# Performance work log

Measured on AMD Instinct MI355X. Metric: run time of the kernel, lower is better.

Reference implementation:

```python
import math
import jax, jax.numpy as jnp
import numpy as np
from jax import lax

# ---- static config (mirrors RPN init + typical torchvision anchor setup) ----
IMG_H = IMG_W = 800
LEVELS = [(200, 200, 4, 32), (100, 100, 8, 64), (50, 50, 16, 128), (25, 25, 32, 256), (13, 13, 64, 512)]  # (h, w, stride, anchor_size)
RATIOS = (0.5, 1.0, 2.0)
COUNTS = tuple(h * w * len(RATIOS) for (h, w, _, _) in LEVELS)  # (120000,30000,7500,1875,507)
A_TOTAL = sum(COUNTS)  # 159882
PRE_NMS = 2000
POST_NMS = 1000
NMS_THRESH = 0.7
MIN_SIZE = 1e-3
BBOX_CLIP = math.log(1000.0 / 16)


def make_anchors():
    parts = []
    for (h, w, stride, size) in LEVELS:
        ws = np.array([size * np.sqrt(1.0 / r) for r in RATIOS], np.float32)  # [3]
        hs = np.array([size * np.sqrt(r) for r in RATIOS], np.float32)
        sx = (np.arange(w, dtype=np.float32) + 0.5) * stride
        sy = (np.arange(h, dtype=np.float32) + 0.5) * stride
        cy, cx = np.meshgrid(sy, sx, indexing='ij')
        cx = cx.reshape(-1, 1)
        cy = cy.reshape(-1, 1)
        a = np.stack([cx - ws / 2, cy - hs / 2, cx + ws / 2, cy + hs / 2], axis=-1)  # [HW,3,4]
        parts.append(a.reshape(-1, 4))
    return np.concatenate(parts, 0).astype(np.float32)


def setup_inputs() -> dict:
    key = jax.random.key(0)
    k1, k2 = jax.random.split(key)
    scores = jax.random.normal(k1, (1, A_TOTAL), dtype=jnp.float32)
    deltas = jax.random.normal(k2, (A_TOTAL, 4), dtype=jnp.float32) * 0.5
    anchors = jnp.asarray(make_anchors())
    return {'scores': scores, 'deltas': deltas, 'anchors': anchors}


def _pairwise_iou(b):
    area = (b[:, 2] - b[:, 0]) * (b[:, 3] - b[:, 1])  # [K]
    lt = jnp.maximum(b[:, None, :2], b[None, :, :2])   # [K,K,2]
    rb = jnp.minimum(b[:, None, 2:], b[None, :, 2:])
    wh = jnp.maximum(rb - lt, 0.0)
    inter = wh[..., 0] * wh[..., 1]
    return inter / (area[:, None] + area[None, :] - inter)


def reference(scores, deltas, anchors):
    s_all = lax.stop_gradient(scores[0])  # original does cls.detach()
    # ---- box decode (torchvision-style) ----
    w = anchors[:, 2] - anchors[:, 0]
    h = anchors[:, 3] - anchors[:, 1]
    cx = anchors[:, 0] + 0.5 * w
    cy = anchors[:, 1] + 0.5 * h
    dx, dy = deltas[:, 0], deltas[:, 1]
    dw = jnp.minimum(deltas[:, 2], BBOX_CLIP)
    dh = jnp.minimum(deltas[:, 3], BBOX_CLIP)
    px = cx + dx * w
    py = cy + dy * h
    pw = jnp.exp(dw) * w
    ph = jnp.exp(dh) * h
    boxes = jnp.stack([px - 0.5 * pw, py - 0.5 * ph, px + 0.5 * pw, py + 0.5 * ph], axis=1)  # [A,4]
    # ---- per-level top-k over objectness ----
    idx_parts = []
    off = 0
    for c in COUNTS:
        k = min(PRE_NMS, c)
        _, ti = lax.top_k(lax.dynamic_slice_in_dim(s_all, off, c), k)
        idx_parts.append(ti + off)
        off += c
    top_idx = jnp.concatenate(idx_parts)  # [K=8382]
    K = top_idx.shape[0]
    s = s_all[top_idx]
    b = boxes[top_idx]
    # ---- clip to image + min-size validity (masked instead of compacted) ----
    b = jnp.stack([jnp.clip(b[:, 0], 0.0, IMG_W), jnp.clip(b[:, 1], 0.0, IMG_H),
                   jnp.clip(b[:, 2], 0.0, IMG_W), jnp.clip(b[:, 3], 0.0, IMG_H)], axis=1)
    valid = ((b[:, 2] - b[:, 0]) >= MIN_SIZE) & ((b[:, 3] - b[:, 1]) >= MIN_SIZE)
    # ---- per-level NMS offset; replicates original feature_mask[keep] indexing
    # (positional indexing into the full anchor-order level-id vector) ----
    fmask_full = np.concatenate([np.full(c, i, np.float32) for i, c in enumerate(COUNTS)])
    fmask = jnp.asarray(fmask_full[:K])
    box_max = jnp.max(jnp.where(valid[:, None], b, -jnp.inf))
    bn = b + (fmask * (box_max + 1.0))[:, None]
    # ---- greedy NMS on score-sorted candidates ----
    s_m = jnp.where(valid, s, -jnp.inf)
    order = jnp.argsort(-s_m)
    s_srt = s_m[order]
    b_srt = b[order]
    iou = _pairwise_iou(bn[order])  # [K,K] ~281MB
    ar = jnp.arange(K)

    def body(i, keep):
        sup = (iou[i] > NMS_THRESH) & (ar > i)
        return jnp.where(keep[i], keep & ~sup, keep)

    keep = lax.fori_loop(0, K, body, s_srt > -jnp.inf)
    final = jnp.where(keep, s_srt, -jnp.inf)
    out_s, oidx = lax.top_k(final, POST_NMS)  # top post_nms kept, score order; -inf pads
    out_b = b_srt[oidx]
    return out_b, out_s
```

## Files before the change

### kernel.cpp

```cpp
#include <hip/hip_runtime.h>
#include <math.h>

typedef unsigned int u32;
typedef unsigned long long u64;
typedef unsigned char u8;

#define K_TOT 8382
#define NCH 131
#define CAP 1024
#define EC 64
#define DC 8
#define GCAP 32768
#define IMGSZ 800.0f

__device__ __constant__ int LOFF[5] = {0, 120000, 150000, 157500, 159375};
__device__ __constant__ int LCNT[5] = {120000, 30000, 7500, 1875, 507};
__device__ __constant__ int KSEL[5] = {2000, 2000, 2000, 1875, 507};
__device__ __constant__ int SELB[5] = {0, 2000, 4000, 6000, 7875};
__device__ __constant__ int HBS[4] = {0, 118, 148, 156};
__device__ __constant__ int GBS[6] = {0, 118, 148, 156, 158, 159};

static __device__ __forceinline__ u32 fkey(float x) {
    u32 u = __float_as_uint(x);
    u32 m = (u32)(((int)u) >> 31) | 0x80000000u;
    return u ^ m;
}

static __device__ __forceinline__ int lvl_of(int s) {
    return (s < 2000) ? 0 : (s < 4000) ? 1 : (s < 6000) ? 2 : (s < 7875) ? 3 : 4;
}

static __device__ __forceinline__ u32 rdl32(u32 v, int j) {
    return (u32)__builtin_amdgcn_readlane((int)v, j);
}
static __device__ __forceinline__ u64 rdlane64(u64 v, int j) {
    u32 lo = (u32)__builtin_amdgcn_readlane((int)(u32)v, j);
    u32 hi = (u32)__builtin_amdgcn_readlane((int)(u32)(v >> 32), j);
    return ((u64)hi << 32) | (u64)lo;
}

static __device__ __forceinline__ u32 wor32(u32 x) {
    x |= (u32)__builtin_amdgcn_update_dpp(0, (int)x, 0x111, 0xf, 0xf, true);
    x |= (u32)__builtin_amdgcn_update_dpp(0, (int)x, 0x112, 0xf, 0xf, true);
    x |= (u32)__builtin_amdgcn_update_dpp(0, (int)x, 0x114, 0xf, 0xf, true);
    x |= (u32)__builtin_amdgcn_update_dpp(0, (int)x, 0x118, 0xf, 0xf, true);
    x |= (u32)__builtin_amdgcn_update_dpp(0, (int)x, 0x142, 0xa, 0xf, true);
    x |= (u32)__builtin_amdgcn_update_dpp(0, (int)x, 0x143, 0xc, 0xf, true);
    return x;
}

static __device__ __forceinline__ u64 pullkeep(u64 k0, u64 k1, u64 k2, u32 sch) {
    int bidx = (int)((sch & 63u) << 2);
    u32 a0l = (u32)__builtin_amdgcn_ds_bpermute(bidx, (int)(u32)k0);
    u32 a0h = (u32)__builtin_amdgcn_ds_bpermute(bidx, (int)(u32)(k0 >> 32));
    u32 a1l = (u32)__builtin_amdgcn_ds_bpermute(bidx, (int)(u32)k1);
    u32 a1h = (u32)__builtin_amdgcn_ds_bpermute(bidx, (int)(u32)(k1 >> 32));
    u32 a2l = (u32)__builtin_amdgcn_ds_bpermute(bidx, (int)(u32)k2);
    u32 a2h = (u32)__builtin_amdgcn_ds_bpermute(bidx, (int)(u32)(k2 >> 32));
    return (sch < 64) ? (((u64)a0h << 32) | (u64)a0l)
         : (sch < 128) ? (((u64)a1h << 32) | (u64)a1l)
                       : (((u64)a2h << 32) | (u64)a2l);
}

static __device__ __forceinline__ void thresh_scan(const u32* hist, u32* scanbuf, int m,
                                                   u32 need, u32* sv, int t) {
    for (int i = t; i < m; i += 1024) scanbuf[i] = hist[m - 1 - i];
    __syncthreads();
    for (int ofs = 1; ofs < m; ofs <<= 1) {
        int i0 = t, i1 = t + 1024;
        u32 a0 = 0, a1 = 0;
        if (i0 < m && i0 >= ofs) a0 = scanbuf[i0 - ofs];
        if (i1 < m && i1 >= ofs) a1 = scanbuf[i1 - ofs];
        __syncthreads();
        if (i0 < m && i0 >= ofs) scanbuf[i0] += a0;
        if (i1 < m && i1 >= ofs) scanbuf[i1] += a1;
        __syncthreads();
    }
    for (int i = t; i < m; i += 1024) {
        u32 inc = scanbuf[i];
        u32 exc = i ? scanbuf[i - 1] : 0;
        if (inc >= need && exc < need) { sv[0] = (u32)(m - 1 - i); sv[1] = need - exc; }
    }
    __syncthreads();
}

__global__ __launch_bounds__(1024) void k_hist(const float* __restrict__ scores,
                                               u32* __restrict__ hist3) {
    __shared__ u32 lh[2048];
    int t = threadIdx.x;
    lh[t] = 0; lh[t + 1024] = 0;
    __syncthreads();
    int b = blockIdx.x;
    int l = (b < HBS[1]) ? 0 : (b < HBS[2]) ? 1 : 2;
    int i = (b - HBS[l]) * 1024 + t;
    if (i < LCNT[l]) atomicAdd(&lh[fkey(scores[LOFF[l] + i]) >> 21], 1u);
    __syncthreads();
    u32* h = hist3 + l * 2048;
    if (lh[t]) atomicAdd(&h[t], lh[t]);
    if (lh[t + 1024]) atomicAdd(&h[t + 1024], lh[t + 1024]);
}

__global__ __launch_bounds__(1024) void k_thresh(const u32* __restrict__ hist3,
                                                 u32* __restrict__ tinfo) {
    __shared__ u32 scanbuf[2048];
    __shared__ u32 sv[2];
    int l = blockIdx.x;
    int t = threadIdx.x;
    thresh_scan(hist3 + l * 2048, scanbuf, 2048, (u32)KSEL[l], sv, t);
    if (t == 0) { tinfo[l * 2] = sv[0]; tinfo[l * 2 + 1] = sv[1]; }
}

__global__ __launch_bounds__(1024) void k_gather(const float* __restrict__ scores,
                                                 const u32* __restrict__ tinfo,
                                                 u32* __restrict__ sel, u32* __restrict__ cgt,
                                                 u32* __restrict__ gcnt, u32* __restrict__ gidx,
                                                 u32* __restrict__ gkey) {
    int b = blockIdx.x;
    int l = (b < GBS[1]) ? 0 : (b < GBS[2]) ? 1 : (b < GBS[3]) ? 2 : (b < GBS[4]) ? 3 : 4;
    int i = (b - GBS[l]) * 1024 + threadIdx.x;
    if (i >= LCNT[l]) return;
    int off = LOFF[l], sb = SELB[l];
    if (l >= 3) { sel[sb + i] = (u32)(off + i); return; }
    u32 ky = fkey(scores[off + i]);
    u32 b1 = tinfo[l * 2];
    u32 top = ky >> 21;
    if (top > b1) {
        u32 p = atomicAdd(&cgt[l], 1u);
        sel[sb + p] = (u32)(off + i);
    } else if (top == b1) {
        u32 e = atomicAdd(&gcnt[l], 1u);
        if (e < GCAP) { gidx[l * GCAP + e] = (u32)i; gkey[l * GCAP + e] = ky; }
    }
}

__global__ __launch_bounds__(1024) void k_final(const u32* __restrict__ gidx,
                                                const u32* __restrict__ gkey,
                                                const u32* __restrict__ gcnt,
                                                const u32* __restrict__ tinfo,
                                                u32* __restrict__ sel) {
    __shared__ u32 hist[2048];
    __shared__ u32 scanbuf[2048];
    __shared__ u32 eqbuf[1024];
    __shared__ u32 sv[2];
    __shared__ u32 c2, ceq;
    int l = blockIdx.x;
    int t = threadIdx.x;
    int k = KSEL[l], sb = SELB[l], off = LOFF[l];
    u32 m = gcnt[l]; if (m > GCAP) m = GCAP;
    u32 b1 = tinfo[l * 2];
    u32 need = tinfo[l * 2 + 1];
    const u32* kb = gkey + l * GCAP;
    const u32* ib = gidx + l * GCAP;
    hist[t] = 0; hist[t + 1024] = 0; __syncthreads();
    for (u32 e = t; e < m; e += 1024) atomicAdd(&hist[(kb[e] >> 10) & 2047u], 1u);
    __syncthreads();
    thresh_scan(hist, scanbuf, 2048, need, sv, t);
    u32 b2 = sv[0], need2 = sv[1];
    __syncthreads();
    hist[t] = 0; __syncthreads();
    for (u32 e = t; e < m; e += 1024) {
        u32 ky = kb[e];
        if (((ky >> 10) & 2047u) == b2) atomicAdd(&hist[ky & 1023u], 1u);
    }
    __syncthreads();
    thresh_scan(hist, scanbuf, 1024, need2, sv, t);
    u32 T = (b1 << 21) | (b2 << 10) | sv[0];
    u32 take = sv[1];
    if (t == 0) { c2 = 0; ceq = 0; }
    __syncthreads();
    u32 nGTbin = need - take;
    u32 base2 = (u32)sb + (u32)k - need;
    for (u32 e = t; e < m; e += 1024) {
        u32 ky = kb[e];
        if (ky > T) { u32 p = atomicAdd(&c2, 1u); sel[base2 + p] = (u32)off + ib[e]; }
        else if (ky == T) { u32 q = atomicAdd(&ceq, 1u); if (q < 1024) eqbuf[q] = ib[e]; }
    }
    __syncthreads();
    if (t == 0) {
        int n = (ceq > 1024u) ? 1024 : (int)ceq;
        for (int a = 1; a < n; ++a) {
            u32 v = eqbuf[a]; int bq = a - 1;
            while (bq >= 0 && eqbuf[bq] > v) { eqbuf[bq + 1] = eqbuf[bq]; --bq; }
            eqbuf[bq + 1] = v;
        }
        for (u32 q = 0; q < take; ++q) sel[base2 + nGTbin + q] = (u32)off + eqbuf[q];
    }
}

__global__ void k_decode(const float* __restrict__ scores, const float4* __restrict__ deltas,
                         const float4* __restrict__ anchors, const u32* __restrict__ sel,
                         float4* __restrict__ candB, float* __restrict__ candS,
                         u32* __restrict__ candV, u32* __restrict__ candA) {
    int s = blockIdx.x * 256 + threadIdx.x;
    if (s >= K_TOT) return;
    u32 a = sel[s];
    float4 an = anchors[a];
    float4 dl = deltas[a];
    float sc = scores[a];
    float w = __fsub_rn(an.z, an.x), h = __fsub_rn(an.w, an.y);
    float cx = __fadd_rn(an.x, __fmul_rn(0.5f, w));
    float cy = __fadd_rn(an.y, __fmul_rn(0.5f, h));
    const float CLIPV = (float)4.1351665567423563;
    float dw = fminf(dl.z, CLIPV);
    float dh = fminf(dl.w, CLIPV);
    float px = __fadd_rn(cx, __fmul_rn(dl.x, w));
    float py = __fadd_rn(cy, __fmul_rn(dl.y, h));
    float pw = __fmul_rn((float)exp((double)dw), w);
    float ph = __fmul_rn((float)exp((double)dh), h);
    float x1 = __fsub_rn(px, __fmul_rn(0.5f, pw));
    float y1 = __fsub_rn(py, __fmul_rn(0.5f, ph));
    float x2 = __fadd_rn(px, __fmul_rn(0.5f, pw));
    float y2 = __fadd_rn(py, __fmul_rn(0.5f, ph));
    x1 = fminf(fmaxf(x1, 0.0f), IMGSZ);
    y1 = fminf(fmaxf(y1, 0.0f), IMGSZ);
    x2 = fminf(fmaxf(x2, 0.0f), IMGSZ);
    y2 = fminf(fmaxf(y2, 0.0f), IMGSZ);
    bool valid = (__fsub_rn(x2, x1) >= 0.001f) && (__fsub_rn(y2, y1) >= 0.001f);
    candB[s] = make_float4(x1, y1, x2, y2);
    candS[s] = sc;
    candV[s] = valid ? 1u : 0u;
    candA[s] = a;
}

__global__ __launch_bounds__(256) void k_rank_lvl(const float* __restrict__ candS,
                                                  const u32* __restrict__ candA,
                                                  u32* __restrict__ Praw) {
    __shared__ u64 tile[256];
    int l = blockIdx.z;
    int cnt = KSEL[l], base = SELB[l];
    int tx = blockIdx.x * 256;
    int ty = blockIdx.y * 256;
    if (tx >= cnt || ty >= cnt) return;
    int t = threadIdx.x;
    u64 Aj = ~0ull;
    if (tx + t < cnt) {
        int j = base + tx + t;
        Aj = ((u64)(~fkey(candS[j])) << 32) | (u64)candA[j];
    }
    tile[t] = Aj;
    __syncthreads();
    int si = ty + t;
    if (si >= cnt) return;
    int s = base + si;
    u64 A = ((u64)(~fkey(candS[s])) << 32) | (u64)candA[s];
    int r = 0;
#pragma unroll 8
    for (int q = 0; q < 256; ++q) r += (tile[q] < A);
    if (r) atomicAdd(&Praw[s], (u32)r);
}

__global__ __launch_bounds__(256) void k_rank_glob(const float* __restrict__ candS,
                                                   const u32* __restrict__ candV,
                                                   const u32* __restrict__ Praw,
                                                   u32* __restrict__ rank) {
    __shared__ u64 colB[256];
    int t = threadIdx.x;
    int cj = blockIdx.x * 256 + t;
    u64 B = ~0ull;
    if (cj < K_TOT) {
        u32 smk = candV[cj] ? fkey(candS[cj]) : 0x007FFFFFu;
        u32 Pj = (u32)SELB[lvl_of(cj)] + Praw[cj];
        B = ((u64)(~smk) << 32) | (u64)Pj;
    }
    colB[t] = B;
    __syncthreads();
    int s = blockIdx.y * 256 + t;
    if (s >= K_TOT) return;
    u32 smk = candV[s] ? fkey(candS[s]) : 0x007FFFFFu;
    u32 Ps = (u32)SELB[lvl_of(s)] + Praw[s];
    u64 myB = ((u64)(~smk) << 32) | (u64)Ps;
    int cnt = 0;
#pragma unroll 8
    for (int j = 0; j < 256; ++j) cnt += (colB[j] < myB);
    if (cnt) atomicAdd(&rank[s], (u32)cnt);
}

__global__ void k_scatter(const float4* __restrict__ candB, const float* __restrict__ candS,
                          const u32* __restrict__ candV, const u32* __restrict__ rank,
                          float4* __restrict__ sB, float* __restrict__ sArea,
                          float* __restrict__ sS, u32* __restrict__ sV) {
    int s = blockIdx.x * 256 + threadIdx.x;
    if (s >= K_TOT) return;
    u32 r = rank[s];
    float4 b = candB[s];
    float area = __fmul_rn(__fsub_rn(b.z, b.x), __fsub_rn(b.w, b.y));
    sB[r] = b; sArea[r] = area; sS[r] = candS[s]; sV[r] = candV[s];
}

__global__ __launch_bounds__(256) void k_mask(const float4* __restrict__ sB,
                                              const float* __restrict__ sArea,
                                              const u32* __restrict__ sV,
                                              u64* __restrict__ vwords,
                                              u64* __restrict__ diag, u32* __restrict__ ecnt,
                                              ulonglong2* __restrict__ epack,
                                              u32* __restrict__ dcnt, u64* __restrict__ dmask,
                                              ulonglong2* __restrict__ dpack) {
    __shared__ float4 cb[64];
    __shared__ float ca[64];
    int wd = blockIdx.x;
    int t = threadIdx.x;
    if (t < 64) {
        int j = wd * 64 + t;
        if (j < K_TOT) { cb[t] = sB[j]; ca[t] = sArea[j]; }
        else { cb[t] = make_float4(0.f, 0.f, 0.f, 0.f); ca[t] = 0.f; }
    }
    __syncthreads();
    int i = blockIdx.y * 256 + t;
    if (i >= K_TOT) return;
    int dwr = i >> 6;
    if (wd < dwr) return;
    float4 bi = sB[i];
    float ai = sArea[i];
    u64 bits = 0;
    int jbase = wd * 64;
    for (int j2 = 0; j2 < 64; ++j2) {
        int j = jbase + j2;
        if (j > i && j < K_TOT) {
            float4 bj = cb[j2];
            float ltx = fmaxf(bi.x, bj.x), lty = fmaxf(bi.y, bj.y);
            float rbx = fminf(bi.z, bj.z), rby = fminf(bi.w, bj.w);
            float wx = fmaxf(__fsub_rn(rbx, ltx), 0.0f);
            float wy = fmaxf(__fsub_rn(rby, lty), 0.0f);
            float inter = __fmul_rn(wx, wy);
            if (inter > 0.0f) {
                float uni = __fsub_rn(__fadd_rn(ai, ca[j2]), inter);
                float iou = inter / uni;
                if (iou > 0.7f) bits |= (1ull << j2);
            }
        }
    }
    if (wd == dwr) {
        diag[i] = bits;
        u64 vb = __ballot(sV[i] != 0u);
        if ((i & 63) == 0) vwords[wd] = vb;
        if (bits != 0ull) {
            u32 p = atomicAdd(&dcnt[dwr], 1u);
            if (p < DC) dpack[dwr * DC + p] = make_ulonglong2((u64)(i & 63), bits);
            atomicOr(&dmask[dwr], 1ull << (i & 63));
        }
    } else if (bits != 0ull) {
        u32 p = atomicAdd(&ecnt[wd], 1u);
        if (p < CAP) epack[wd * CAP + p] = make_ulonglong2((u64)i, bits);
    }
}

__global__ __launch_bounds__(1024) void k_scan(const u64* __restrict__ diag,
                                               const u64* __restrict__ vwords,
                                               const u32* __restrict__ ecnt,
                                               const ulonglong2* __restrict__ tpack,
                                               const u32* __restrict__ dcnt,
                                               const u64* __restrict__ dmask,
                                               const ulonglong2* __restrict__ dpack,
                                               const float4* __restrict__ sB,
                                               const float* __restrict__ sS,
                                               float* __restrict__ out) {
    __shared__ ulonglong2 sTpack[NCH * EC];
    __shared__ ulonglong2 sDpack[NCH * DC];
    __shared__ u64 sKeep[NCH];
    __shared__ u32 pc[NCH + 1];
    int t = threadIdx.x;
    int w = t >> 6, lane = t & 63;
    {
        int e0 = t, e1 = t + 1024, e2 = t + 2048, e3 = t + 3072, e4 = t + 4096;
        int e5 = t + 5120, e6 = t + 6144, e7 = t + 7168, e8 = t + 8192;
        bool p8 = e8 < NCH * EC;
        ulonglong2 a0 = tpack[(size_t)(e0 >> 6) * CAP + (e0 & 63)];
        ulonglong2 a1 = tpack[(size_t)(e1 >> 6) * CAP + (e1 & 63)];
        ulonglong2 a2 = tpack[(size_t)(e2 >> 6) * CAP + (e2 & 63)];
        ulonglong2 a3 = tpack[(size_t)(e3 >> 6) * CAP + (e3 & 63)];
        ulonglong2 a4 = tpack[(size_t)(e4 >> 6) * CAP + (e4 & 63)];
        ulonglong2 a5 = tpack[(size_t)(e5 >> 6) * CAP + (e5 & 63)];
        ulonglong2 a6 = tpack[(size_t)(e6 >> 6) * CAP + (e6 & 63)];
        ulonglong2 a7 = tpack[(size_t)(e7 >> 6) * CAP + (e7 & 63)];
        ulonglong2 a8 = make_ulonglong2(0ull, 0ull);
        if (p8) a8 = tpack[(size_t)(e8 >> 6) * CAP + (e8 & 63)];
        sTpack[e0] = a0; sTpack[e1] = a1; sTpack[e2] = a2; sTpack[e3] = a3;
        sTpack[e4] = a4; sTpack[e5] = a5; sTpack[e6] = a6; sTpack[e7] = a7;
        if (p8) sTpack[e8] = a8;
    }
    {
        ulonglong2 a0, a1;
        bool p1 = (t + 1024) < NCH * DC;
        a0 = dpack[t];
        if (p1) a1 = dpack[t + 1024];
        sDpack[t] = a0;
        if (p1) sDpack[t + 1024] = a1;
    }
    u64 v0 = 0, v1 = 0, v2 = 0, m0 = 0, m1 = 0, m2 = 0;
    u32 c0 = 0, c1 = 0, c2 = 0, d0 = 0, d1 = 0, d2 = 0;
    if (w == 0) {
        int i0 = lane, i1 = lane + 64, i2 = lane + 128;
        bool p2 = (i2 < NCH);
        v0 = vwords[i0]; v1 = vwords[i1]; v2 = p2 ? vwords[i2] : 0;
        c0 = ecnt[i0]; c1 = ecnt[i1]; c2 = p2 ? ecnt[i2] : 0;
        d0 = dcnt[i0]; d1 = dcnt[i1]; d2 = p2 ? dcnt[i2] : 0;
        m0 = dmask[i0]; m1 = dmask[i1]; m2 = p2 ? dmask[i2] : 0;
        if (c0 > CAP) c0 = CAP;
        if (c1 > CAP) c1 = CAP;
        if (c2 > CAP) c2 = CAP;
    }
    __syncthreads();
    if (w == 0) {
        u64 k0 = 0, k1 = 0, k2 = 0;
        ulonglong2 E = sTpack[lane];
        ulonglong2 DP = (lane < DC) ? sDpack[lane] : make_ulonglong2(~0ull, 0ull);
        u32 cnt = rdl32(c0, 0), dn = rdl32(d0, 0);
        u64 vw = rdlane64(v0, 0), dmw = rdlane64(m0, 0);
        for (int c = 0; c < NCH; ++c) {
            int cn = (c + 1 < NCH) ? (c + 1) : c;
            ulonglong2 En = sTpack[cn * EC + lane];
            ulonglong2 DPn = (lane < DC) ? sDpack[cn * DC + lane] : make_ulonglong2(~0ull, 0ull);
            u32 cntn, dnn; u64 vwn, dmn;
            if (cn < 64)       { cntn = rdl32(c0, cn);       dnn = rdl32(d0, cn);       vwn = rdlane64(v0, cn);       dmn = rdlane64(m0, cn); }
            else if (cn < 128) { cntn = rdl32(c1, cn - 64);  dnn = rdl32(d1, cn - 64);  vwn = rdlane64(v1, cn - 64);  dmn = rdlane64(m1, cn - 64); }
            else               { cntn = rdl32(c2, cn - 128); dnn = rdl32(d2, cn - 128); vwn = rdlane64(v2, cn - 128); dmn = rdlane64(m2, cn - 128); }
            u64 incoming = 0;
            if (cnt) {
                u64 mbits = 0;
                {
                    u32 sidx = (u32)E.x & 0x3FFFu;
                    u64 kw = pullkeep(k0, k1, k2, sidx >> 6);
                    if (((u32)lane < cnt) && ((kw >> (sidx & 63u)) & 1ull)) mbits = E.y;
                }
                if (cnt > (u32)EC) {
                    for (u32 e = (u32)EC + (u32)lane; e < cnt; e += 64u) {
                        ulonglong2 Et = tpack[(size_t)c * CAP + e];
                        u32 sidx = (u32)Et.x & 0x3FFFu;
                        u64 kw = pullkeep(k0, k1, k2, sidx >> 6);
                        if ((kw >> (sidx & 63u)) & 1ull) mbits |= Et.y;
                    }
                }
                u32 lo = wor32((u32)mbits);
                u32 hi = wor32((u32)(mbits >> 32));
                incoming = ((u64)rdl32(hi, 63) << 32) | (u64)rdl32(lo, 63);
            }
            u64 alive = vw & ~incoming;
            if (dn) {
                if (dn <= (u32)DC) {
                    u64 dm = dmw & alive;
                    u32 ml = ((u32)lane < dn) ? (u32)DP.x : 0xFFu;
                    while (dm) {
                        int j = __builtin_ctzll(dm);
                        dm &= dm - 1;
                        if ((alive >> j) & 1ull) {
                            u64 selm = __ballot(ml == (u32)j);
                            int src = __builtin_ctzll(selm);
                            alive &= ~rdlane64(DP.y, src);
                        }
                    }
                } else {
                    int r = c * 64 + lane;
                    u64 D = (r < K_TOT) ? diag[r] : 0ull;
                    u64 nzd = __ballot(D != 0ull);
                    nzd &= alive;
                    while (nzd) {
                        int j = __builtin_ctzll(nzd);
                        nzd &= nzd - 1;
                        if ((alive >> j) & 1ull) alive &= ~rdlane64(D, j);
                    }
                }
            }
            if (lane == 0) sKeep[c] = alive;
            if (c < 64)       { if (lane == c)       k0 = alive; }
            else if (c < 128) { if (lane == c - 64)  k1 = alive; }
            else              { if (lane == c - 128) k2 = alive; }
            E = En; DP = DPn; cnt = cntn; dn = dnn; vw = vwn; dmw = dmn;
        }
    }
    __syncthreads();
    if (t < NCH) pc[t + 1] = (u32)__popcll(sKeep[t]);
    if (t == 0) pc[0] = 0;
    __syncthreads();
    for (int ofs = 1; ofs < NCH; ofs <<= 1) {
        int i = t + 1;
        u32 v = 0;
        bool p = (t < NCH) && (i - ofs >= 1);
        if (p) v = pc[i - ofs];
        __syncthreads();
        if (p) pc[i] += v;
        __syncthreads();
    }
    u32 nk = pc[NCH];
    for (int i = t; i < K_TOT; i += 1024) {
        int wi = i >> 6, b = i & 63;
        u64 kw = sKeep[wi];
        u32 kb = pc[wi] + (u32)__popcll(kw & ((1ull << b) - 1ull));
        bool kp = (kw >> b) & 1ull;
        if (kp) {
            if (kb < 1000u) {
                float4 bx = sB[i];
                out[kb * 4 + 0] = bx.x; out[kb * 4 + 1] = bx.y;
                out[kb * 4 + 2] = bx.z; out[kb * 4 + 3] = bx.w;
                out[4000 + kb] = sS[i];
            }
        } else {
            u32 q = (u32)i - kb;
            u32 slot = nk + q;
            if (slot < 1000u) {
                float4 bx = sB[i];
                out[slot * 4 + 0] = bx.x; out[slot * 4 + 1] = bx.y;
                out[slot * 4 + 2] = bx.z; out[slot * 4 + 3] = bx.w;
                out[4000 + slot] = -INFINITY;
            }
        }
    }
}

static constexpr size_t al256(size_t x) { return (x + 255) & ~(size_t)255; }
static constexpr size_t KB4 = (size_t)K_TOT * 4;
static constexpr size_t KB16 = (size_t)K_TOT * 16;
static constexpr size_t O_RANK = 0;
static constexpr size_t O_PRAW = al256(O_RANK + KB4);
static constexpr size_t O_ECNT = al256(O_PRAW + KB4);
static constexpr size_t O_DCNT = al256(O_ECNT + (size_t)NCH * 4);
static constexpr size_t O_DMASK = al256(O_DCNT + (size_t)NCH * 4);
static constexpr size_t O_HIST = al256(O_DMASK + (size_t)NCH * 8);
static constexpr size_t O_CGT = al256(O_HIST + (size_t)3 * 2048 * 4);
static constexpr size_t O_GCNT = al256(O_CGT + 3 * 4);
static constexpr size_t MEMSET_BYTES = al256(O_GCNT + 3 * 4);
static constexpr size_t O_TINFO = MEMSET_BYTES;
static constexpr size_t O_SEL = al256(O_TINFO + 6 * 4);
static constexpr size_t O_GIDX = al256(O_SEL + KB4);
static constexpr size_t O_GKEY = al256(O_GIDX + (size_t)3 * GCAP * 4);
static constexpr size_t O_CANDB = al256(O_GKEY + (size_t)3 * GCAP * 4);
static constexpr size_t O_CANDS = al256(O_CANDB + KB16);
static constexpr size_t O_CANDV = al256(O_CANDS + KB4);
static constexpr size_t O_CANDA = al256(O_CANDV + KB4);
static constexpr size_t O_SB = al256(O_CANDA + KB4);
static constexpr size_t O_SAREA = al256(O_SB + KB16);
static constexpr size_t O_SS = al256(O_SAREA + KB4);
static constexpr size_t O_SV = al256(O_SS + KB4);
static constexpr size_t O_VW = al256(O_SV + KB4);
static constexpr size_t O_DIAG = al256(O_VW + (size_t)NCH * 8);
static constexpr size_t O_EPACK = al256(O_DIAG + (size_t)(NCH * 64) * 8);
static constexpr size_t O_DPACK = al256(O_EPACK + (size_t)NCH * CAP * 16);

extern "C" void kernel_launch(void* const* d_in, const int* in_sizes, int n_in,
                              void* d_out, int out_size, void* d_ws, size_t ws_size,
                              hipStream_t stream) {
    const float* scores = (const float*)d_in[0];
    const float4* deltas = (const float4*)d_in[1];
    const float4* anchors = (const float4*)d_in[2];
    float* out = (float*)d_out;
    char* ws = (char*)d_ws;

    u32* rank = (u32*)(ws + O_RANK);
    u32* Praw = (u32*)(ws + O_PRAW);
    u32* ecnt = (u32*)(ws + O_ECNT);
    u32* dcnt = (u32*)(ws + O_DCNT);
    u64* dmask = (u64*)(ws + O_DMASK);
    u32* hist3 = (u32*)(ws + O_HIST);
    u32* cgt = (u32*)(ws + O_CGT);
    u32* gcnt = (u32*)(ws + O_GCNT);
    u32* tinfo = (u32*)(ws + O_TINFO);
    u32* sel = (u32*)(ws + O_SEL);
    u32* gidx = (u32*)(ws + O_GIDX);
    u32* gkey = (u32*)(ws + O_GKEY);
    float4* candB = (float4*)(ws + O_CANDB);
    float* candS = (float*)(ws + O_CANDS);
    u32* candV = (u32*)(ws + O_CANDV);
    u32* candA = (u32*)(ws + O_CANDA);
    float4* sB = (float4*)(ws + O_SB);
    float* sArea = (float*)(ws + O_SAREA);
    float* sS = (float*)(ws + O_SS);
    u32* sV = (u32*)(ws + O_SV);
    u64* vwords = (u64*)(ws + O_VW);
    u64* diag = (u64*)(ws + O_DIAG);
    ulonglong2* epack = (ulonglong2*)(ws + O_EPACK);
    ulonglong2* dpack = (ulonglong2*)(ws + O_DPACK);

    hipMemsetAsync(ws, 0, MEMSET_BYTES, stream);

    const int NBLK = (K_TOT + 255) / 256;
    k_hist<<<156, 1024, 0, stream>>>(scores, hist3);
    k_thresh<<<3, 1024, 0, stream>>>(hist3, tinfo);
    k_gather<<<159, 1024, 0, stream>>>(scores, tinfo, sel, cgt, gcnt, gidx, gkey);
    k_final<<<3, 1024, 0, stream>>>(gidx, gkey, gcnt, tinfo, sel);
    k_decode<<<NBLK, 256, 0, stream>>>(scores, deltas, anchors, sel, candB, candS, candV, candA);
    k_rank_lvl<<<dim3(8, 8, 5), 256, 0, stream>>>(candS, candA, Praw);
    k_rank_glob<<<dim3(NBLK, NBLK), 256, 0, stream>>>(candS, candV, Praw, rank);
    k_scatter<<<NBLK, 256, 0, stream>>>(candB, candS, candV, rank, sB, sArea, sS, sV);
    k_mask<<<dim3(NCH, NBLK), 256, 0, stream>>>(sB, sArea, sV, vwords, diag, ecnt, epack, dcnt, dmask, dpack);
    k_scan<<<1, 1024, 0, stream>>>(diag, vwords, ecnt, epack, dcnt, dmask, dpack, sB, sS, out);
}
```

Before: 213.2 us.

## Restructure serial NMS scan to compute next chunk's suppression early and drop dpack

The single-wave greedy NMS scan now computes the incoming suppression mask for chunk c+1 right after chunk c's keep word is final, and prefetches sTpack and diag rows two chunks ahead. Keep words are read from a shared array instead of bpermute across lane registers. The diagonal packing (dcnt/dpack with atomics) is replaced by a ballot-written dmask and direct reads of diag rows. This is meant to shorten the serial dependency chain per chunk, at the cost of more global diag loads inside the loop and a different memset layout, where dmask is no longer zeroed but is always written.

Result: no change. 212.9 us (-0.1%).

```diff
diff --git a/kernel.cpp b/kernel.cpp
--- a/kernel.cpp
+++ b/kernel.cpp
@@ -9,7 +9,6 @@
 #define NCH 131
 #define CAP 1024
 #define EC 64
-#define DC 8
 #define GCAP 32768
 #define IMGSZ 800.0f
 
@@ -47,19 +46,6 @@
     x |= (u32)__builtin_amdgcn_update_dpp(0, (int)x, 0x142, 0xa, 0xf, true);
     x |= (u32)__builtin_amdgcn_update_dpp(0, (int)x, 0x143, 0xc, 0xf, true);
     return x;
-}
-
-static __device__ __forceinline__ u64 pullkeep(u64 k0, u64 k1, u64 k2, u32 sch) {
-    int bidx = (int)((sch & 63u) << 2);
-    u32 a0l = (u32)__builtin_amdgcn_ds_bpermute(bidx, (int)(u32)k0);
-    u32 a0h = (u32)__builtin_amdgcn_ds_bpermute(bidx, (int)(u32)(k0 >> 32));
-    u32 a1l = (u32)__builtin_amdgcn_ds_bpermute(bidx, (int)(u32)k1);
-    u32 a1h = (u32)__builtin_amdgcn_ds_bpermute(bidx, (int)(u32)(k1 >> 32));
-    u32 a2l = (u32)__builtin_amdgcn_ds_bpermute(bidx, (int)(u32)k2);
-    u32 a2h = (u32)__builtin_amdgcn_ds_bpermute(bidx, (int)(u32)(k2 >> 32));
-    return (sch < 64) ? (((u64)a0h << 32) | (u64)a0l)
-         : (sch < 128) ? (((u64)a1h << 32) | (u64)a1l)
-                       : (((u64)a2h << 32) | (u64)a2l);
 }
 
 static __device__ __forceinline__ void thresh_scan(const u32* hist, u32* scanbuf, int m,
@@ -293,8 +279,7 @@
                                               u64* __restrict__ vwords,
                                               u64* __restrict__ diag, u32* __restrict__ ecnt,
                                               ulonglong2* __restrict__ epack,
-                                              u32* __restrict__ dcnt, u64* __restrict__ dmask,
-                                              ulonglong2* __restrict__ dpack) {
+                                              u64* __restrict__ dmask) {
     __shared__ float4 cb[64];
     __shared__ float ca[64];
     int wd = blockIdx.x;
@@ -332,12 +317,8 @@
     if (wd == dwr) {
         diag[i] = bits;
         u64 vb = __ballot(sV[i] != 0u);
-        if ((i & 63) == 0) vwords[wd] = vb;
-        if (bits != 0ull) {
-            u32 p = atomicAdd(&dcnt[dwr], 1u);
-            if (p < DC) dpack[dwr * DC + p] = make_ulonglong2((u64)(i & 63), bits);
-            atomicOr(&dmask[dwr], 1ull << (i & 63));
-        }
+        u64 db = __ballot(bits != 0ull);
+        if ((i & 63) == 0) { vwords[wd] = vb; dmask[wd] = db; }
     } else if (bits != 0ull) {
         u32 p = atomicAdd(&ecnt[wd], 1u);
         if (p < CAP) epack[wd * CAP + p] = make_ulonglong2((u64)i, bits);
@@ -348,15 +329,12 @@
                                                const u64* __restrict__ vwords,
                                                const u32* __restrict__ ecnt,
                                                const ulonglong2* __restrict__ tpack,
-                                               const u32* __restrict__ dcnt,
                                                const u64* __restrict__ dmask,
-                                               const ulonglong2* __restrict__ dpack,
                                                const float4* __restrict__ sB,
                                                const float* __restrict__ sS,
                                                float* __restrict__ out) {
     __shared__ ulonglong2 sTpack[NCH * EC];
-    __shared__ ulonglong2 sDpack[NCH * DC];
-    __shared__ u64 sKeep[NCH];
+    __shared__ u64 sKeepArr[NCH];
     __shared__ u32 pc[NCH + 1];
     int t = threadIdx.x;
     int w = t >> 6, lane = t & 63;
@@ -378,22 +356,13 @@
         sTpack[e4] = a4; sTpack[e5] = a5; sTpack[e6] = a6; sTpack[e7] = a7;
         if (p8) sTpack[e8] = a8;
     }
-    {
-        ulonglong2 a0, a1;
-        bool p1 = (t + 1024) < NCH * DC;
-        a0 = dpack[t];
-        if (p1) a1 = dpack[t + 1024];
-        sDpack[t] = a0;
-        if (p1) sDpack[t + 1024] = a1;
-    }
     u64 v0 = 0, v1 = 0, v2 = 0, m0 = 0, m1 = 0, m2 = 0;
-    u32 c0 = 0, c1 = 0, c2 = 0, d0 = 0, d1 = 0, d2 = 0;
+    u32 c0 = 0, c1 = 0, c2 = 0;
     if (w == 0) {
         int i0 = lane, i1 = lane + 64, i2 = lane + 128;
         bool p2 = (i2 < NCH);
         v0 = vwords[i0]; v1 = vwords[i1]; v2 = p2 ? vwords[i2] : 0;
         c0 = ecnt[i0]; c1 = ecnt[i1]; c2 = p2 ? ecnt[i2] : 0;
-        d0 = dcnt[i0]; d1 = dcnt[i1]; d2 = p2 ? dcnt[i2] : 0;
         m0 = dmask[i0]; m1 = dmask[i1]; m2 = p2 ? dmask[i2] : 0;
         if (c0 > CAP) c0 = CAP;
         if (c1 > CAP) c1 = CAP;
@@ -401,74 +370,68 @@
     }
     __syncthreads();
     if (w == 0) {
-        u64 k0 = 0, k1 = 0, k2 = 0;
-        ulonglong2 E = sTpack[lane];
-        ulonglong2 DP = (lane < DC) ? sDpack[lane] : make_ulonglong2(~0ull, 0ull);
-        u32 cnt = rdl32(c0, 0), dn = rdl32(d0, 0);
+        ulonglong2 Ea = sTpack[EC + lane];
+        u64 Dcur = diag[lane];
+        u64 Dnx  = diag[64 + lane];
         u64 vw = rdlane64(v0, 0), dmw = rdlane64(m0, 0);
+        u64 inc = 0;
+        u32 cntn = rdl32(c0, 1);
         for (int c = 0; c < NCH; ++c) {
-            int cn = (c + 1 < NCH) ? (c + 1) : c;
-            ulonglong2 En = sTpack[cn * EC + lane];
-            ulonglong2 DPn = (lane < DC) ? sDpack[cn * DC + lane] : make_ulonglong2(~0ull, 0ull);
-            u32 cntn, dnn; u64 vwn, dmn;
-            if (cn < 64)       { cntn = rdl32(c0, cn);       dnn = rdl32(d0, cn);       vwn = rdlane64(v0, cn);       dmn = rdlane64(m0, cn); }
-            else if (cn < 128) { cntn = rdl32(c1, cn - 64);  dnn = rdl32(d1, cn - 64);  vwn = rdlane64(v1, cn - 64);  dmn = rdlane64(m1, cn - 64); }
-            else               { cntn = rdl32(c2, cn - 128); dnn = rdl32(d2, cn - 128); vwn = rdlane64(v2, cn - 128); dmn = rdlane64(m2, cn - 128); }
-            u64 incoming = 0;
-            if (cnt) {
-                u64 mbits = 0;
-                {
-                    u32 sidx = (u32)E.x & 0x3FFFu;
-                    u64 kw = pullkeep(k0, k1, k2, sidx >> 6);
-                    if (((u32)lane < cnt) && ((kw >> (sidx & 63u)) & 1ull)) mbits = E.y;
-                }
-                if (cnt > (u32)EC) {
-                    for (u32 e = (u32)EC + (u32)lane; e < cnt; e += 64u) {
-                        ulonglong2 Et = tpack[(size_t)c * CAP + e];
-                        u32 sidx = (u32)Et.x & 0x3FFFu;
-                        u64 kw = pullkeep(k0, k1, k2, sidx >> 6);
-                        if ((kw >> (sidx & 63u)) & 1ull) mbits |= Et.y;
-                    }
-                }
-                u32 lo = wor32((u32)mbits);
-                u32 hi = wor32((u32)(mbits >> 32));
-                incoming = ((u64)rdl32(hi, 63) << 32) | (u64)rdl32(lo, 63);
-            }
-            u64 alive = vw & ~incoming;
-            if (dn) {
-                if (dn <= (u32)DC) {
-                    u64 dm = dmw & alive;
-                    u32 ml = ((u32)lane < dn) ? (u32)DP.x : 0xFFu;
-                    while (dm) {
-                        int j = __builtin_ctzll(dm);
-                        dm &= dm - 1;
-                        if ((alive >> j) & 1ull) {
-                            u64 selm = __ballot(ml == (u32)j);
-                            int src = __builtin_ctzll(selm);
-                            alive &= ~rdlane64(DP.y, src);
-                        }
-                    }
-                } else {
-                    int r = c * 64 + lane;
-                    u64 D = (r < K_TOT) ? diag[r] : 0ull;
-                    u64 nzd = __ballot(D != 0ull);
-                    nzd &= alive;
-                    while (nzd) {
-                        int j = __builtin_ctzll(nzd);
-                        nzd &= nzd - 1;
-                        if ((alive >> j) & 1ull) alive &= ~rdlane64(D, j);
+            int cn  = (c + 1 < NCH) ? (c + 1) : c;
+            int cn2 = (c + 2 < NCH) ? (c + 2) : c;
+            ulonglong2 Eb = sTpack[cn2 * EC + lane];
+            u64 Dnn = diag[cn2 * 64 + lane];
+            u32 sidx = (u32)Ea.x;
+            u32 sch = sidx >> 6;
+            u64 Kw = sKeepArr[(sch < (u32)NCH) ? sch : 0];
+            u32 cntn2; u64 vwn, dmn;
+            if (cn < 64)       { vwn = rdlane64(v0, cn);       dmn = rdlane64(m0, cn); }
+            else if (cn < 128) { vwn = rdlane64(v1, cn - 64);  dmn = rdlane64(m1, cn - 64); }
+            else               { vwn = rdlane64(v2, cn - 128); dmn = rdlane64(m2, cn - 128); }
+            if (cn2 < 64)       cntn2 = rdl32(c0, cn2);
+            else if (cn2 < 128) cntn2 = rdl32(c1, cn2 - 64);
+            else                cntn2 = rdl32(c2, cn2 - 128);
+            u64 alive = vw & ~inc;
+            if (dmw) {
+                u64 dm = dmw & alive;
+                while (dm) {
+                    int j = __builtin_ctzll(dm);
+                    dm &= dm - 1;
+                    if ((alive >> j) & 1ull) {
+                        alive &= ~rdlane64(Dcur, j);
+                        dm &= alive;
                     }
                 }
             }
-            if (lane == 0) sKeep[c] = alive;
-            if (c < 64)       { if (lane == c)       k0 = alive; }
-            else if (c < 128) { if (lane == c - 64)  k1 = alive; }
-            else              { if (lane == c - 128) k2 = alive; }
-            E = En; DP = DPn; cnt = cntn; dn = dnn; vw = vwn; dmw = dmn;
+            if (lane == 0) sKeepArr[c] = alive;
+            u64 m = 0;
+            if ((u32)lane < cntn) {
+                u64 kw2 = (sch == (u32)c) ? alive : Kw;
+                if ((kw2 >> (sidx & 63u)) & 1ull) m = Ea.y;
+            }
+            u32 lo = wor32((u32)m);
+            u32 hi = wor32((u32)(m >> 32));
+            u64 incn = ((u64)rdl32(hi, 63) << 32) | (u64)rdl32(lo, 63);
+            if (cntn > (u32)EC) {
+                u64 mt = 0;
+                for (u32 e = (u32)EC + (u32)lane; e < cntn; e += 64u) {
+                    ulonglong2 Et = tpack[(size_t)cn * CAP + e];
+                    u32 si = (u32)Et.x;
+                    u32 sc2 = si >> 6;
+                    u64 kw3 = (sc2 == (u32)c) ? alive : sKeepArr[sc2];
+                    if ((kw3 >> (si & 63u)) & 1ull) mt |= Et.y;
+                }
+                lo = wor32((u32)mt);
+                hi = wor32((u32)(mt >> 32));
+                incn |= ((u64)rdl32(hi, 63) << 32) | (u64)rdl32(lo, 63);
+            }
+            inc = incn;
+            Ea = Eb; Dcur = Dnx; Dnx = Dnn;
+            vw = vwn; dmw = dmn; cntn = cntn2;
         }
     }
     __syncthreads();
-    if (t < NCH) pc[t + 1] = (u32)__popcll(sKeep[t]);
+    if (t < NCH) pc[t + 1] = (u32)__popcll(sKeepArr[t]);
     if (t == 0) pc[0] = 0;
     __syncthreads();
     for (int ofs = 1; ofs < NCH; ofs <<= 1) {
@@ -483,7 +446,7 @@
     u32 nk = pc[NCH];
     for (int i = t; i < K_TOT; i += 1024) {
         int wi = i >> 6, b = i & 63;
-        u64 kw = sKeep[wi];
+        u64 kw = sKeepArr[wi];
         u32 kb = pc[wi] + (u32)__popcll(kw & ((1ull << b) - 1ull));
         bool kp = (kw >> b) & 1ull;
         if (kp) {
@@ -512,9 +475,7 @@
 static constexpr size_t O_RANK = 0;
 static constexpr size_t O_PRAW = al256(O_RANK + KB4);
 static constexpr size_t O_ECNT = al256(O_PRAW + KB4);
-static constexpr size_t O_DCNT = al256(O_ECNT + (size_t)NCH * 4);
-static constexpr size_t O_DMASK = al256(O_DCNT + (size_t)NCH * 4);
-static constexpr size_t O_HIST = al256(O_DMASK + (size_t)NCH * 8);
+static constexpr size_t O_HIST = al256(O_ECNT + (size_t)NCH * 4);
 static constexpr size_t O_CGT = al256(O_HIST + (size_t)3 * 2048 * 4);
 static constexpr size_t O_GCNT = al256(O_CGT + 3 * 4);
 static constexpr size_t MEMSET_BYTES = al256(O_GCNT + 3 * 4);
@@ -531,9 +492,9 @@
 static constexpr size_t O_SS = al256(O_SAREA + KB4);
 static constexpr size_t O_SV = al256(O_SS + KB4);
 static constexpr size_t O_VW = al256(O_SV + KB4);
-static constexpr size_t O_DIAG = al256(O_VW + (size_t)NCH * 8);
+static constexpr size_t O_DMASK = al256(O_VW + (size_t)NCH * 8);
+static constexpr size_t O_DIAG = al256(O_DMASK + (size_t)NCH * 8);
 static constexpr size_t O_EPACK = al256(O_DIAG + (size_t)(NCH * 64) * 8);
-static constexpr size_t O_DPACK = al256(O_EPACK + (size_t)NCH * CAP * 16);
 
 extern "C" void kernel_launch(void* const* d_in, const int* in_sizes, int n_in,
                               void* d_out, int out_size, void* d_ws, size_t ws_size,
@@ -547,8 +508,6 @@
     u32* rank = (u32*)(ws + O_RANK);
     u32* Praw = (u32*)(ws + O_PRAW);
     u32* ecnt = (u32*)(ws + O_ECNT);
-    u32* dcnt = (u32*)(ws + O_DCNT);
-    u64* dmask = (u64*)(ws + O_DMASK);
     u32* hist3 = (u32*)(ws + O_HIST);
     u32* cgt = (u32*)(ws + O_CGT);
     u32* gcnt = (u32*)(ws + O_GCNT);
@@ -565,9 +524,9 @@
     float* sS = (float*)(ws + O_SS);
     u32* sV = (u32*)(ws + O_SV);
     u64* vwords = (u64*)(ws + O_VW);
+    u64* dmask = (u64*)(ws + O_DMASK);
     u64* diag = (u64*)(ws + O_DIAG);
     ulonglong2* epack = (ulonglong2*)(ws + O_EPACK);
-    ulonglong2* dpack = (ulonglong2*)(ws + O_DPACK);
 
     hipMemsetAsync(ws, 0, MEMSET_BYTES, stream);
 
@@ -580,6 +539,6 @@
     k_rank_lvl<<<dim3(8, 8, 5), 256, 0, stream>>>(candS, candA, Praw);
     k_rank_glob<<<dim3(NBLK, NBLK), 256, 0, stream>>>(candS, candV, Praw, rank);
     k_scatter<<<NBLK, 256, 0, stream>>>(candB, candS, candV, rank, sB, sArea, sS, sV);
-    k_mask<<<dim3(NCH, NBLK), 256, 0, stream>>>(sB, sArea, sV, vwords, diag, ecnt, epack, dcnt, dmask, dpack);
-    k_scan<<<1, 1024, 0, stream>>>(diag, vwords, ecnt, epack, dcnt, dmask, dpack, sB, sS, out);
-}
+    k_mask<<<dim3(NCH, NBLK), 256, 0, stream>>>(sB, sArea, sV, vwords, diag, ecnt, epack, dmask);
+    k_scan<<<1, 1024, 0, stream>>>(diag, vwords, ecnt, epack, dmask, sB, sS, out);
+}
```
